# Kernel optimization log

Measured on AMD Instinct MI355X. Metric: run time of the kernel, lower is better.

The kernel has to match this reference:

```python
import jax, jax.numpy as jnp
import numpy as np
from jax import lax


def setup_inputs() -> dict:
    key = jax.random.key(0)
    k1, k2, k3 = jax.random.split(key, 3)
    B, F, L = 16384, 1024, 3
    x = jax.random.normal(k1, (B, F), dtype=jnp.float32)
    # xavier_uniform on [F,1]: bound = sqrt(6/(F+1))
    bound = float(np.sqrt(6.0 / (F + 1)))
    kernels = jax.random.uniform(k2, (L, F, 1), dtype=jnp.float32, minval=-bound, maxval=bound)
    bias = jax.random.uniform(k3, (L, F, 1), dtype=jnp.float32, minval=-bound, maxval=bound)
    return {"x": x, "kernels": kernels, "bias": bias}


def reference(x, kernels, bias):
    # DCN vector cross: xl_{i+1} = x0 * (xl . w_i) + b_i + xl
    x0 = x  # [B, F]

    def step(xl, wb):
        w, b = wb  # w: [F,1], b: [F,1]
        s = xl @ w[:, 0]                     # [B]  (xl^T w per batch row)
        xl_new = x0 * s[:, None] + b[:, 0] + xl  # [B, F]
        return xl_new, None

    xl, _ = lax.scan(step, x0, (kernels, bias))
    return xl
```

## Files before the change

### kernel.cpp

```cpp
#include <hip/hip_runtime.h>


constexpr int B = 16384;
constexpr int F = 1024;
constexpr int WAVES = 4;
constexpr int ROWS_PER_BLOCK = WAVES;
constexpr int BLOCK = 64 * WAVES;

__global__ __launch_bounds__(BLOCK) void prep_kernel(
    const float* __restrict__ kernels,
    const float* __restrict__ bias,
    float* __restrict__ ws)
{
    const int tid = threadIdx.x;
    const float4* w1v = (const float4*)(kernels + F);
    const float4* w2v = (const float4*)(kernels + 2 * F);
    const float4* b0v = (const float4*)(bias);
    const float4* b1v = (const float4*)(bias + F);
    const float4* b2v = (const float4*)(bias + 2 * F);

    const float4 B0 = b0v[tid];
    const float4 B1 = b1v[tid];
    const float4 B2 = b2v[tid];
    float4 bs;
    bs.x = B0.x + B1.x + B2.x;
    bs.y = B0.y + B1.y + B2.y;
    bs.z = B0.z + B1.z + B2.z;
    bs.w = B0.w + B1.w + B2.w;
    ((float4*)(ws + 4))[tid] = bs;

    if (tid < 64) {
        float t01 = 0.f, t02 = 0.f, t12 = 0.f;
#pragma unroll
        for (int c = 0; c < 4; ++c) {
            const int i = c * 64 + tid;
            const float4 w1 = w1v[i];
            const float4 w2 = w2v[i];
            const float4 b0 = b0v[i];
            const float4 b1 = b1v[i];
            t01 = fmaf(b0.x, w1.x, t01); t01 = fmaf(b0.y, w1.y, t01);
            t01 = fmaf(b0.z, w1.z, t01); t01 = fmaf(b0.w, w1.w, t01);
            t02 = fmaf(b0.x, w2.x, t02); t02 = fmaf(b0.y, w2.y, t02);
            t02 = fmaf(b0.z, w2.z, t02); t02 = fmaf(b0.w, w2.w, t02);
            t12 = fmaf(b1.x, w2.x, t12); t12 = fmaf(b1.y, w2.y, t12);
            t12 = fmaf(b1.z, w2.z, t12); t12 = fmaf(b1.w, w2.w, t12);
        }
#pragma unroll
        for (int off = 32; off >= 1; off >>= 1) {
            t01 += __shfl_xor(t01, off, 64);
            t02 += __shfl_xor(t02, off, 64);
            t12 += __shfl_xor(t12, off, 64);
        }
        if (tid == 0) {
            ws[0] = t01;
            ws[1] = t02;
            ws[2] = t12;
        }
    }
}

__global__ __launch_bounds__(BLOCK) void cross_layer_kernel(
    const float* __restrict__ x,
    const float* __restrict__ kernels,
    const float* __restrict__ ws,
    float* __restrict__ out)
{
    const int lane = threadIdx.x & 63;
    const int wave = threadIdx.x >> 6;
    const int row  = blockIdx.x * ROWS_PER_BLOCK + wave;

    const float4* xrow = (const float4*)(x + (size_t)row * F);
    const float4* w0v  = (const float4*)(kernels);
    const float4* w1v  = (const float4*)(kernels + F);
    const float4* w2v  = (const float4*)(kernels + 2 * F);
    const float4* bsv  = (const float4*)(ws + 4);

    float4 x0[4];
#pragma unroll
    for (int c = 0; c < 4; ++c) x0[c] = xrow[c * 64 + lane];

    const float t01  = ws[0];
    const float tsum = ws[1] + ws[2];

    float d0 = 0.f, d1 = 0.f, d2 = 0.f;
#pragma unroll
    for (int c = 0; c < 4; ++c) {
        const int i = c * 64 + lane;
        const float4 w0 = w0v[i];
        const float4 w1 = w1v[i];
        const float4 w2 = w2v[i];
        const float4 xv = x0[c];
        d0 = fmaf(xv.x, w0.x, d0); d0 = fmaf(xv.y, w0.y, d0);
        d0 = fmaf(xv.z, w0.z, d0); d0 = fmaf(xv.w, w0.w, d0);
        d1 = fmaf(xv.x, w1.x, d1); d1 = fmaf(xv.y, w1.y, d1);
        d1 = fmaf(xv.z, w1.z, d1); d1 = fmaf(xv.w, w1.w, d1);
        d2 = fmaf(xv.x, w2.x, d2); d2 = fmaf(xv.y, w2.y, d2);
        d2 = fmaf(xv.z, w2.z, d2); d2 = fmaf(xv.w, w2.w, d2);
    }

#pragma unroll
    for (int off = 32; off >= 1; off >>= 1) {
        d0 += __shfl_xor(d0, off, 64);
        d1 += __shfl_xor(d1, off, 64);
        d2 += __shfl_xor(d2, off, 64);
    }

    const float a1 = 1.f + d0;
    const float s1 = fmaf(a1, d1, t01);
    const float a2 = a1 + s1;
    const float s2 = fmaf(a2, d2, tsum);
    const float S  = a2 + s2;

    float4* orow = (float4*)(out + (size_t)row * F);
#pragma unroll
    for (int c = 0; c < 4; ++c) {
        const int i = c * 64 + lane;
        const float4 bs = bsv[i];
        float4 o;
        o.x = fmaf(x0[c].x, S, bs.x);
        o.y = fmaf(x0[c].y, S, bs.y);
        o.z = fmaf(x0[c].z, S, bs.z);
        o.w = fmaf(x0[c].w, S, bs.w);
        orow[i] = o;
    }
}

extern "C" void kernel_launch(void* const* d_in, const int* in_sizes, int n_in,
                              void* d_out, int out_size, void* d_ws, size_t ws_size,
                              hipStream_t stream) {
    const float* x       = (const float*)d_in[0];
    const float* kernels = (const float*)d_in[1];
    const float* bias    = (const float*)d_in[2];
    float* out           = (float*)d_out;
    float* ws            = (float*)d_ws;

    prep_kernel<<<dim3(1), dim3(BLOCK), 0, stream>>>(kernels, bias, ws);
    cross_layer_kernel<<<dim3(B / ROWS_PER_BLOCK), dim3(BLOCK), 0, stream>>>(
        x, kernels, ws, out);
}
```

Baseline: 120.8 us.

## Split fused cross kernel into reduction pass and streaming elementwise pass

The single fused kernel, which loaded each row, reduced three dot products and wrote the output, becomes two kernels. The first computes the per-row scalar S and stores it in workspace. The second streams x again and writes x*S + bias with a flat per-thread indexing scheme. This reads x twice from memory and adds a launch, trading that extra traffic for simpler, more streaming-friendly kernels. The 64 MB input may not stay in cache between passes, so it risks more memory traffic on a bandwidth-bound problem.

```diff
diff --git a/kernel.cpp b/kernel.cpp
--- a/kernel.cpp
+++ b/kernel.cpp
@@ -3,9 +3,7 @@
 
 constexpr int B = 16384;
 constexpr int F = 1024;
-constexpr int WAVES = 4;
-constexpr int ROWS_PER_BLOCK = WAVES;
-constexpr int BLOCK = 64 * WAVES;
+constexpr int BLOCK = 256;
 
 __global__ __launch_bounds__(BLOCK) void prep_kernel(
     const float* __restrict__ kernels,
@@ -51,45 +49,32 @@
             t02 += __shfl_xor(t02, off, 64);
             t12 += __shfl_xor(t12, off, 64);
         }
-        if (tid == 0) {
-            ws[0] = t01;
-            ws[1] = t02;
-            ws[2] = t12;
-        }
+        if (tid == 0) { ws[0] = t01; ws[1] = t02; ws[2] = t12; }
     }
 }
 
-__global__ __launch_bounds__(BLOCK) void cross_layer_kernel(
+__global__ __launch_bounds__(BLOCK) void pass1_kernel(
     const float* __restrict__ x,
     const float* __restrict__ kernels,
-    const float* __restrict__ ws,
-    float* __restrict__ out)
+    float* __restrict__ ws)
 {
     const int lane = threadIdx.x & 63;
     const int wave = threadIdx.x >> 6;
-    const int row  = blockIdx.x * ROWS_PER_BLOCK + wave;
+    const int row  = blockIdx.x * 4 + wave;
 
     const float4* xrow = (const float4*)(x + (size_t)row * F);
     const float4* w0v  = (const float4*)(kernels);
     const float4* w1v  = (const float4*)(kernels + F);
     const float4* w2v  = (const float4*)(kernels + 2 * F);
-    const float4* bsv  = (const float4*)(ws + 4);
-
-    float4 x0[4];
-#pragma unroll
-    for (int c = 0; c < 4; ++c) x0[c] = xrow[c * 64 + lane];
-
-    const float t01  = ws[0];
-    const float tsum = ws[1] + ws[2];
 
     float d0 = 0.f, d1 = 0.f, d2 = 0.f;
 #pragma unroll
     for (int c = 0; c < 4; ++c) {
         const int i = c * 64 + lane;
+        const float4 xv = xrow[i];
         const float4 w0 = w0v[i];
         const float4 w1 = w1v[i];
         const float4 w2 = w2v[i];
-        const float4 xv = x0[c];
         d0 = fmaf(xv.x, w0.x, d0); d0 = fmaf(xv.y, w0.y, d0);
         d0 = fmaf(xv.z, w0.z, d0); d0 = fmaf(xv.w, w0.w, d0);
         d1 = fmaf(xv.x, w1.x, d1); d1 = fmaf(xv.y, w1.y, d1);
@@ -105,23 +90,44 @@
         d2 += __shfl_xor(d2, off, 64);
     }
 
-    const float a1 = 1.f + d0;
-    const float s1 = fmaf(a1, d1, t01);
-    const float a2 = a1 + s1;
-    const float s2 = fmaf(a2, d2, tsum);
-    const float S  = a2 + s2;
+    if (lane == 0) {
+        const float t01  = ws[0];
+        const float tsum = ws[1] + ws[2];
+        const float a1 = 1.f + d0;
+        const float s1 = fmaf(a1, d1, t01);
+        const float a2 = a1 + s1;
+        const float s2 = fmaf(a2, d2, tsum);
+        ws[2048 + row] = a2 + s2;
+    }
+}
 
-    float4* orow = (float4*)(out + (size_t)row * F);
+__global__ __launch_bounds__(BLOCK) void pass2_kernel(
+    const float* __restrict__ x,
+    const float* __restrict__ ws,
+    float* __restrict__ out)
+{
+    const int tid  = blockIdx.x * BLOCK + threadIdx.x;
+    const int wid  = tid >> 6;
+    const int lane = tid & 63;
+
+    const float4* xv  = (const float4*)x;
+    float4*       ov  = (float4*)out;
+    const float4* bsv = (const float4*)(ws + 4);
+    const float*  Sp  = ws + 2048;
+
 #pragma unroll
-    for (int c = 0; c < 4; ++c) {
-        const int i = c * 64 + lane;
-        const float4 bs = bsv[i];
+    for (int k = 0; k < 8; ++k) {
+        const int i   = wid * 512 + k * 64 + lane;
+        const int row = i >> 8;
+        const float  s  = Sp[row];
+        const float4 xq = xv[i];
+        const float4 bs = bsv[i & 255];
         float4 o;
-        o.x = fmaf(x0[c].x, S, bs.x);
-        o.y = fmaf(x0[c].y, S, bs.y);
-        o.z = fmaf(x0[c].z, S, bs.z);
-        o.w = fmaf(x0[c].w, S, bs.w);
-        orow[i] = o;
+        o.x = fmaf(xq.x, s, bs.x);
+        o.y = fmaf(xq.y, s, bs.y);
+        o.z = fmaf(xq.z, s, bs.z);
+        o.w = fmaf(xq.w, s, bs.w);
+        ov[i] = o;
     }
 }
 
@@ -135,6 +141,6 @@
     float* ws            = (float*)d_ws;
 
     prep_kernel<<<dim3(1), dim3(BLOCK), 0, stream>>>(kernels, bias, ws);
-    cross_layer_kernel<<<dim3(B / ROWS_PER_BLOCK), dim3(BLOCK), 0, stream>>>(
-        x, kernels, ws, out);
+    pass1_kernel<<<dim3(B / 4), dim3(BLOCK), 0, stream>>>(x, kernels, ws);
+    pass2_kernel<<<dim3(2048), dim3(BLOCK), 0, stream>>>(x, ws, out);
 }
```

Measured after the change: 124.0 us. 1.03x slower.
